# Optimization experiments

Measured on AMD Instinct MI355X. Metric: run time of the kernel, lower is better.

The kernel has to match this reference:

```python
import jax, jax.numpy as jnp
import numpy as np

B, T, D, H = 4, 3072, 1024, 16
HD = D // H

def setup_inputs() -> dict:
    key = jax.random.key(0)
    ks = jax.random.split(key, 7)
    s = 1.0 / np.sqrt(D)
    x = jax.random.normal(ks[0], (B, T, D), dtype=jnp.float32)
    Wq = jax.random.normal(ks[1], (D, D), dtype=jnp.float32) * s
    Wk = jax.random.normal(ks[2], (D, D), dtype=jnp.float32) * s
    Wv = jax.random.normal(ks[3], (D, D), dtype=jnp.float32) * s
    Wo = jax.random.normal(ks[4], (D, D), dtype=jnp.float32) * s
    bo = jnp.zeros((D,), dtype=jnp.float32)
    Wconv = jax.random.normal(ks[5], (D, D, 3), dtype=jnp.float32) * (1.0 / np.sqrt(3 * D))  # (out, in, kw)
    return {"x": x, "Wq": Wq, "Wk": Wk, "Wv": Wv, "Wo": Wo, "bo": bo, "Wconv": Wconv}

def reference(x, Wq, Wk, Wv, Wo, bo, Wconv):
    b, t, d = x.shape
    # stride-3 conv pooling of K/V stream (Conv1d(D, D, 3, stride=3, bias=False))
    kc = jax.lax.conv_general_dilated(
        x.transpose(0, 2, 1), Wconv, window_strides=(3,), padding='VALID',
        dimension_numbers=('NCH', 'OIH', 'NCH')).transpose(0, 2, 1)  # (B, T//3, D)
    k_tmp = jnp.concatenate([x[:, :1, :], kc], axis=1)  # (B, Tk, D)
    tk = k_tmp.shape[1]
    # comparison-based bias mask: masked where 3*k_idx >= q_idx + 0.001
    q_idx = jnp.arange(t, dtype=jnp.float32)
    k_idx = jnp.arange(tk, dtype=jnp.float32)
    mask = (k_idx[None, :] * 3.0 >= q_idx[:, None] + 0.001).astype(x.dtype)  # (T, Tk)
    # projections (torch Linear: y = x @ W.T)
    q = x @ Wq.T
    k = k_tmp @ Wk.T
    v = k_tmp @ Wv.T
    q = q.reshape(b, t, H, HD).transpose(0, 2, 1, 3)   # (B, H, T, HD)
    k = k.reshape(b, tk, H, HD).transpose(0, 2, 1, 3)  # (B, H, Tk, HD)
    v = v.reshape(b, tk, H, HD).transpose(0, 2, 1, 3)
    scores = jnp.einsum('bhqd,bhkd->bhqk', q, k) * (HD ** -0.5)
    scores = scores + mask * jnp.asarray(-1e9, dtype=x.dtype)
    p = jax.nn.softmax(scores, axis=-1)  # dropout is identity in eval (p=0)
    o = jnp.einsum('bhqk,bhkd->bhqd', p, v)
    o = o.transpose(0, 2, 1, 3).reshape(b, t, d)
    return o @ Wo.T + bo
```

## Files before the change

kernel.cpp:

```cpp
#include <hip/hip_runtime.h>
#include <hip/hip_bf16.h>
#include <cstdint>
#include <cstddef>

typedef __attribute__((ext_vector_type(8))) __bf16 bf16x8;
typedef __attribute__((ext_vector_type(4))) __bf16 bf16x4;
typedef __attribute__((ext_vector_type(4))) float  floatx4;

#define MFMA16x16x32(a, b, c) __builtin_amdgcn_mfma_f32_16x16x32_bf16((a), (b), (c), 0, 0, 0)

#define ATTN_SC 0.18033688011112042f

__device__ __forceinline__ void gload_lds16(const void* g, void* l) {
  __builtin_amdgcn_global_load_lds((const __attribute__((address_space(1))) void*)g,
                                   (__attribute__((address_space(3))) void*)l,
                                   16, 0, 0);
}


__global__ void prep_kernel(const float* __restrict__ x,
                            const float* __restrict__ Wq, const float* __restrict__ Wk,
                            const float* __restrict__ Wv, const float* __restrict__ Wo,
                            const float* __restrict__ Wconv,
                            __bf16* __restrict__ xb,
                            __bf16* __restrict__ wqb, __bf16* __restrict__ wkb,
                            __bf16* __restrict__ wvb, __bf16* __restrict__ wob,
                            __bf16* __restrict__ wc2, __bf16* __restrict__ ktmp) {
  const int bid = blockIdx.x, tid = threadIdx.x;
  if (bid < 4096) {
    const int which = bid >> 10;
    const float* src = (which == 0) ? Wq : (which == 1) ? Wk : (which == 2) ? Wv : Wo;
    __bf16* dst = (which == 0) ? wqb : (which == 1) ? wkb : (which == 2) ? wvb : wob;
    const int i = (bid & 1023) * 256 + tid;
    floatx4 v = *(const floatx4*)(src + (size_t)i * 4);
    bf16x4 o; o[0] = (__bf16)v[0]; o[1] = (__bf16)v[1]; o[2] = (__bf16)v[2]; o[3] = (__bf16)v[3];
    *(bf16x4*)(dst + (size_t)i * 4) = o;
  } else if (bid < 5120) {
    const int t = (bid - 4096) * 256 + tid;
    const int o = t >> 8, c = t & 255;
    const float* base = Wconv + (size_t)o * 3072 + c * 12;
    float f[12];
    *(floatx4*)(f)     = *(const floatx4*)(base);
    *(floatx4*)(f + 4) = *(const floatx4*)(base + 4);
    *(floatx4*)(f + 8) = *(const floatx4*)(base + 8);
#pragma unroll
    for (int kw = 0; kw < 3; ++kw) {
      bf16x4 q;
#pragma unroll
      for (int j = 0; j < 4; ++j) q[j] = (__bf16)f[3 * j + kw];
      *(bf16x4*)(wc2 + (size_t)o * 3072 + kw * 1024 + c * 4) = q;
    }
  } else if (bid < 5136) {
    const int i = (bid - 5120) * 256 + tid;
    const int b = i >> 10, c = i & 1023;
    ktmp[(size_t)b * 1025 * 1024 + c] = (__bf16)x[(size_t)b * 3072 * 1024 + c];
  } else {
    const int i = (bid - 5136) * 256 + tid;
    floatx4 v = *(const floatx4*)(x + (size_t)i * 4);
    bf16x4 o; o[0] = (__bf16)v[0]; o[1] = (__bf16)v[1]; o[2] = (__bf16)v[2]; o[3] = (__bf16)v[3];
    *(bf16x4*)(xb + (size_t)i * 4) = o;
  }
}

__global__ void vtrans_kernel(const __bf16* __restrict__ V, __bf16* __restrict__ Vt) {
  __shared__ __attribute__((aligned(16))) __bf16 tile[64][72];
  const int tid = threadIdx.x;
  const int bh = blockIdx.y;
  const int b = bh >> 4, h = bh & 15;
  const int t0 = blockIdx.x * 64;
  const int r = tid >> 3, s = tid & 7;
#pragma unroll
  for (int p = 0; p < 2; ++p) {
    const int t = p * 32 + r;
    bf16x8 v = *(const bf16x8*)(V + ((size_t)(b * 1025 + t0 + t)) * 1024 + h * 64 + s * 8);
    *(bf16x8*)(&tile[t][s * 8]) = v;
  }
  __syncthreads();
#pragma unroll
  for (int p = 0; p < 2; ++p) {
    const int d = p * 32 + r;
    bf16x8 o;
#pragma unroll
    for (int e = 0; e < 8; ++e) o[e] = tile[s * 8 + e][d];
    *(bf16x8*)(Vt + ((size_t)bh * 64 + d) * 1024 + t0 + s * 8) = o;
  }
}


template <int MODE>
__device__ __forceinline__ void gemm4_body(
    const __bf16* __restrict__ A, const __bf16* __restrict__ Bw, void* __restrict__ Cout,
    const float* __restrict__ bias, int N, int K, int m0, int n0,
    __bf16* As, __bf16* Bs)
{
  const int tid  = threadIdx.x;
  const int wave = tid >> 6;
  const int lane = tid & 63;
  const int g    = lane >> 4;
  const int ln   = lane & 15;
  const int wc   = wave * 64;

  size_t aSrcv[2], bSrcv[4];
#pragma unroll
  for (int q = 0; q < 2; ++q) {
    const int c = tid + q * 256, pr = c >> 3, ca = (c & 7) ^ (pr & 7);
    aSrcv[q] = (size_t)(m0 + pr + ((ca >> 2) << 6)) * K + ((ca & 3) << 3);
  }
#pragma unroll
  for (int q = 0; q < 4; ++q) {
    const int c = tid + q * 256, pr = c >> 3, ca = (c & 7) ^ (pr & 7);
    bSrcv[q] = (size_t)(n0 + pr + ((ca >> 2) << 7)) * K + ((ca & 3) << 3);
  }

  int aOff[8], bOff[4];
#pragma unroll
  for (int i = 0; i < 8; ++i) {
    const int ra = i * 16 + ln;
    const int pr = ra & 63;
    const int c  = ((ra >> 6) << 2) + g;
    aOff[i] = pr * 64 + ((c ^ (pr & 7)) << 3);
  }
#pragma unroll
  for (int j = 0; j < 4; ++j) {
    const int rb = wc + j * 16 + ln;
    const int pr = rb & 127;
    const int c  = ((rb >> 7) << 2) + g;
    bOff[j] = pr * 64 + ((c ^ (pr & 7)) << 3);
  }

  floatx4 acc[8][4];
#pragma unroll
  for (int i = 0; i < 8; ++i)
#pragma unroll
    for (int j = 0; j < 4; ++j) { floatx4 z = {0.f, 0.f, 0.f, 0.f}; acc[i][j] = z; }

  auto STAGE = [&](int t, int s) {
    const int koff = t * 32;
    __bf16* ad = As + s * 4096 + (tid << 3);
    __bf16* bd = Bs + s * 8192 + (tid << 3);
    gload_lds16(A  + aSrcv[0] + koff, ad);
    gload_lds16(A  + aSrcv[1] + koff, ad + 2048);
    gload_lds16(Bw + bSrcv[0] + koff, bd);
    gload_lds16(Bw + bSrcv[1] + koff, bd + 2048);
    gload_lds16(Bw + bSrcv[2] + koff, bd + 4096);
    gload_lds16(Bw + bSrcv[3] + koff, bd + 6144);
  };

  bf16x8 af[8], bf[4];

#define READF(s)                                                                   \
  {                                                                                \
    const __bf16* ah_ = As + (s) * 4096;                                           \
    const __bf16* bh_ = Bs + (s) * 8192;                                           \
    _Pragma("unroll")                                                              \
    for (int i_ = 0; i_ < 8; ++i_) af[i_] = *(const bf16x8*)(ah_ + aOff[i_]);      \
    _Pragma("unroll")                                                              \
    for (int j_ = 0; j_ < 4; ++j_) bf[j_] = *(const bf16x8*)(bh_ + bOff[j_]);      \
  }

#define MFMAC()                                                                    \
  {                                                                                \
    __builtin_amdgcn_s_setprio(1);                                                 \
    _Pragma("unroll")                                                              \
    for (int i_ = 0; i_ < 8; ++i_)                                                 \
      _Pragma("unroll")                                                            \
      for (int j_ = 0; j_ < 4; ++j_)                                               \
        acc[i_][j_] = MFMA16x16x32(af[i_], bf[j_], acc[i_][j_]);                   \
    __builtin_amdgcn_s_setprio(0);                                                 \
  }

  const int HT = K >> 5;

  STAGE(0, 0);
  STAGE(1, 1);
  asm volatile("s_waitcnt vmcnt(6)" ::: "memory");
  __builtin_amdgcn_s_barrier();
  __builtin_amdgcn_sched_barrier(0);

  int sp = 0;
  for (int h = 0; h < HT; ++h) {
    const int s2 = (sp + 2 >= 3) ? sp - 1 : sp + 2;
    READF(sp);
    if (h + 2 < HT) STAGE(h + 2, s2);
    MFMAC();
    if (h + 1 < HT) {
      if (h + 2 < HT) { asm volatile("s_waitcnt vmcnt(6) lgkmcnt(0)" ::: "memory"); }
      else            { asm volatile("s_waitcnt vmcnt(0) lgkmcnt(0)" ::: "memory"); }
      __builtin_amdgcn_s_barrier();
      __builtin_amdgcn_sched_barrier(0);
    }
    sp = (sp + 1 >= 3) ? 0 : sp + 1;
  }

#undef READF
#undef MFMAC

#pragma unroll
  for (int j = 0; j < 4; ++j) {
    const int col = n0 + wc + j * 16 + ln;
    float bj = 0.f;
    if (MODE == 2) bj = bias[col];
#pragma unroll
    for (int i = 0; i < 8; ++i)
#pragma unroll
      for (int r = 0; r < 4; ++r) {
        const int row = m0 + i * 16 + g * 4 + r;
        if (MODE == 2) {
          ((float*)Cout)[(size_t)row * N + col] = acc[i][j][r] + bj;
        } else if (MODE == 1) {
          const size_t orow = (size_t)(row >> 10) * 1025 + 1 + (row & 1023);
          ((__bf16*)Cout)[orow * 1024 + col] = (__bf16)acc[i][j][r];
        } else if (MODE == 4) {
          ((__bf16*)Cout)[(size_t)row * N + col] = (__bf16)(acc[i][j][r] * ATTN_SC);
        } else {
          ((__bf16*)Cout)[(size_t)row * N + col] = (__bf16)acc[i][j][r];
        }
      }
  }
}

__global__ __launch_bounds__(256, 2) void gemm_convq_kernel(
    const __bf16* __restrict__ xb, const __bf16* __restrict__ wc2,
    const __bf16* __restrict__ wqb, __bf16* __restrict__ ktmp, __bf16* __restrict__ qb)
{
  __shared__ __attribute__((aligned(16))) __bf16 As[12288];
  __shared__ __attribute__((aligned(16))) __bf16 Bs[24576];
  const int xcd = blockIdx.x & 7, s = blockIdx.x >> 3;
  if (s < 16) {
    const int id = xcd * 16 + s;
    gemm4_body<1>(xb, wc2, ktmp, nullptr, 1024, 3072, (id >> 2) * 128, (id & 3) * 256, As, Bs);
  } else {
    const int id = xcd * 48 + (s - 16);
    gemm4_body<4>(xb, wqb, qb, nullptr, 1024, 1024, (id >> 2) * 128, (id & 3) * 256, As, Bs);
  }
}

__global__ __launch_bounds__(256, 2) void gemm_kv_kernel(
    const __bf16* __restrict__ ktmp, const __bf16* __restrict__ wkb,
    const __bf16* __restrict__ wvb, __bf16* __restrict__ kb, __bf16* __restrict__ vb)
{
  __shared__ __attribute__((aligned(16))) __bf16 As[12288];
  __shared__ __attribute__((aligned(16))) __bf16 Bs[24576];
  const int id = (blockIdx.x & 7) * 33 + (blockIdx.x >> 3);
  const int p  = (id >= 132) ? 1 : 0;
  const int rest = id - p * 132;
  gemm4_body<0>(ktmp, p ? wvb : wkb, p ? vb : kb, nullptr, 1024, 1024,
                (rest >> 2) * 128, (rest & 3) * 256, As, Bs);
}

__global__ __launch_bounds__(256, 2) void gemm_o_kernel(
    const __bf16* __restrict__ ob, const __bf16* __restrict__ wob,
    float* __restrict__ out, const float* __restrict__ bo)
{
  __shared__ __attribute__((aligned(16))) __bf16 As[12288];
  __shared__ __attribute__((aligned(16))) __bf16 Bs[24576];
  const int id = (blockIdx.x & 7) * 48 + (blockIdx.x >> 3);
  gemm4_body<2>(ob, wob, out, bo, 1024, 1024, (id >> 2) * 128, (id & 3) * 256, As, Bs);
}


__global__ __launch_bounds__(256) void attn_kernel(
    const __bf16* __restrict__ Q, const __bf16* __restrict__ Kk,
    const __bf16* __restrict__ Vt, __bf16* __restrict__ O)
{
  __shared__ __attribute__((aligned(16))) __bf16 Kd[2][64 * 64];
  __shared__ __attribute__((aligned(16))) __bf16 Vd[2][64 * 64];
  __shared__ __attribute__((aligned(16))) __bf16 Ps[4][32 * 64];

  const int tid  = threadIdx.x;
  const int wave = tid >> 6;
  const int lane = tid & 63;
  const int g    = lane >> 4;
  const int ln   = lane & 15;

  const int l    = blockIdx.x;
  const int xcd  = l & 7;
  const int b    = xcd >> 1;
  const int rest = l >> 3;
  const int h    = rest & 15;
  const int qt   = ((11 - (rest >> 4)) << 1) | (xcd & 1);
  const int q0   = qt * 128 + wave * 32;

  const size_t qrow0 = (size_t)b * 3072 + q0;
  const size_t krow0 = (size_t)b * 1025;
  const size_t vtrow = ((size_t)(b * 16 + h)) * 64;
  const int hc = h * 64;
  const int sw = (ln & 7) << 3;
  __bf16* Pw = Ps[wave];

  const int srow = lane >> 3;
  const int scol = (lane & 7) * 8;

  auto stage = [&](int kt, int bb) {
    const int kb0 = kt * 64;
#pragma unroll
    for (int i = 0; i < 2; ++i) {
      const int rr = (wave * 2 + i) * 8 + srow;
      gload_lds16(Kk + (krow0 + kb0 + rr) * 1024 + hc + scol,
                  Kd[bb] + (size_t)rr * 64 + scol);
      gload_lds16(Vt + (vtrow + rr) * 1024 + kb0 + scol,
                  Vd[bb] + (size_t)rr * 64 + scol);
    }
  };

  bf16x8 qf[2][2];
#pragma unroll
  for (int i = 0; i < 2; ++i)
#pragma unroll
    for (int kc = 0; kc < 2; ++kc)
      qf[i][kc] = *(const bf16x8*)(Q + (qrow0 + i * 16 + ln) * 1024 + hc + kc * 32 + g * 8);

  floatx4 oacc[2][4];
  floatx4 oal[2];
#pragma unroll
  for (int i = 0; i < 2; ++i) {
    floatx4 z = {0.f, 0.f, 0.f, 0.f};
    oal[i] = z;
#pragma unroll
    for (int dt = 0; dt < 4; ++dt) oacc[i][dt] = z;
  }

  bf16x8 ones;
#pragma unroll
  for (int e = 0; e < 8; ++e) ones[e] = (__bf16)1.0f;

  const int nkt_blk = (((qt * 128 + 127) / 3) >> 6) + 1;
  const int nfull   = (q0 >= 189) ? ((q0 - 189) / 192 + 1) : 0;

  stage(0, 0);

  for (int kt = 0; kt < nkt_blk; ++kt) {
    const int bb = kt & 1;
    __syncthreads();
    if (kt + 1 < nkt_blk) stage(kt + 1, bb ^ 1);
    const int kb0 = kt * 64;
    const bool masked = (kt >= nfull);

    bf16x8 kf[4][2];
#pragma unroll
    for (int jk = 0; jk < 4; ++jk)
#pragma unroll
      for (int kc = 0; kc < 2; ++kc)
        kf[jk][kc] = *(const bf16x8*)(Kd[bb] + (jk * 16 + ln) * 64 + kc * 32 + g * 8);

#pragma unroll
    for (int jk = 0; jk < 4; ++jk)
#pragma unroll
      for (int i = 0; i < 2; ++i) {
        floatx4 s = {0.f, 0.f, 0.f, 0.f};
        s = MFMA16x16x32(kf[jk][0], qf[i][0], s);
        s = MFMA16x16x32(kf[jk][1], qf[i][1], s);
        float p[4];
#pragma unroll
        for (int r = 0; r < 4; ++r) {
          float e = __builtin_amdgcn_exp2f(s[r]);
          if (masked) {
            const int key = kb0 + jk * 16 + 4 * g + r;
            const int q   = q0 + i * 16 + ln;
            e = (3 * key <= q) ? e : 0.f;
          }
          p[r] = e;
        }
        bf16x4 pk;
        pk[0] = (__bf16)p[0]; pk[1] = (__bf16)p[1]; pk[2] = (__bf16)p[2]; pk[3] = (__bf16)p[3];
        *(bf16x4*)(Pw + (i * 16 + ln) * 64 + ((jk * 16 + 4 * g) ^ sw)) = pk;
      }

#pragma unroll
    for (int kc = 0; kc < 2; ++kc) {
      bf16x8 pf0 = *(const bf16x8*)(Pw + (ln) * 64      + ((kc * 32 + g * 8) ^ sw));
      bf16x8 pf1 = *(const bf16x8*)(Pw + (16 + ln) * 64 + ((kc * 32 + g * 8) ^ sw));
      oal[0] = MFMA16x16x32(ones, pf0, oal[0]);
      oal[1] = MFMA16x16x32(ones, pf1, oal[1]);
#pragma unroll
      for (int dt = 0; dt < 4; ++dt) {
        bf16x8 vf = *(const bf16x8*)(Vd[bb] + (dt * 16 + ln) * 64 + kc * 32 + g * 8);
        oacc[0][dt] = MFMA16x16x32(vf, pf0, oacc[0][dt]);
        oacc[1][dt] = MFMA16x16x32(vf, pf1, oacc[1][dt]);
      }
    }
  }

#pragma unroll
  for (int i = 0; i < 2; ++i) {
    const float inv = 1.0f / oal[i][0];
    const size_t row = qrow0 + i * 16 + ln;
#pragma unroll
    for (int dt = 0; dt < 4; ++dt) {
      bf16x4 o4;
#pragma unroll
      for (int r = 0; r < 4; ++r) o4[r] = (__bf16)(oacc[i][dt][r] * inv);
      *(bf16x4*)(O + row * 1024 + hc + dt * 16 + 4 * g) = o4;
    }
  }
}


extern "C" void kernel_launch(void* const* d_in, const int* in_sizes, int n_in,
                              void* d_out, int out_size, void* d_ws, size_t ws_size,
                              hipStream_t stream) {
  (void)in_sizes; (void)n_in; (void)out_size; (void)ws_size;
  const float* x     = (const float*)d_in[0];
  const float* Wq    = (const float*)d_in[1];
  const float* Wk    = (const float*)d_in[2];
  const float* Wv    = (const float*)d_in[3];
  const float* Wo    = (const float*)d_in[4];
  const float* bo    = (const float*)d_in[5];
  const float* Wconv = (const float*)d_in[6];

  char* ws = (char*)d_ws;
  const size_t SZ_XQ = (size_t)12288 * 1024 * 2;
  const size_t SZ_KT = (size_t)4224 * 1024 * 2;
  const size_t SZ_W  = (size_t)1024 * 1024 * 2;

  __bf16* xb   = (__bf16*)(ws);
  __bf16* qb   = (__bf16*)(ws + SZ_XQ);
  __bf16* ktmp = (__bf16*)(ws + 2 * SZ_XQ);
  __bf16* kb   = (__bf16*)(ws + 2 * SZ_XQ + SZ_KT);
  __bf16* vb   = (__bf16*)(ws + 2 * SZ_XQ + 2 * SZ_KT);
  __bf16* wqb  = (__bf16*)(ws + 2 * SZ_XQ + 3 * SZ_KT);
  __bf16* wkb  = (__bf16*)(ws + 2 * SZ_XQ + 3 * SZ_KT + SZ_W);
  __bf16* wvb  = (__bf16*)(ws + 2 * SZ_XQ + 3 * SZ_KT + 2 * SZ_W);
  __bf16* wob  = (__bf16*)(ws + 2 * SZ_XQ + 3 * SZ_KT + 3 * SZ_W);
  __bf16* wc2  = (__bf16*)(ws + 2 * SZ_XQ + 3 * SZ_KT + 4 * SZ_W);
  __bf16* vt   = xb;

  prep_kernel<<<dim3(17424), dim3(256), 0, stream>>>(x, Wq, Wk, Wv, Wo, Wconv,
                                                     xb, wqb, wkb, wvb, wob, wc2, ktmp);
  gemm_convq_kernel<<<dim3(512), dim3(256), 0, stream>>>(xb, wc2, wqb, ktmp, qb);
  gemm_kv_kernel<<<dim3(264), dim3(256), 0, stream>>>(ktmp, wkb, wvb, kb, vb);
  vtrans_kernel<<<dim3(16, 64), dim3(256), 0, stream>>>(vb, vt);
  attn_kernel<<<dim3(1536), dim3(256), 0, stream>>>(qb, kb, vt, qb);
  gemm_o_kernel<<<dim3(384), dim3(256), 0, stream>>>(qb, wob, (float*)d_out, bo);
}
```

Before: 314.4 us.

## Split conv GEMM K dimension across taps with fp16 partials and reduction

The stride-3 conv GEMM (K=3072) is split into three K=1024 slices, one per tap, so 384 blocks do equal work alongside the 384 Q-projection blocks instead of 128 long blocks. Two taps write fp16 partial sums into reused K/V buffers, and a new reduce kernel adds them into the third tap's bf16 output in ktmp. This targets load imbalance and tail effects in the fused conv+Q launch. The cost is an extra kernel launch, extra memory traffic for the partials, and some rounding from storing partials in fp16 and bf16.

```diff
diff --git a/kernel.cpp b/kernel.cpp
--- a/kernel.cpp
+++ b/kernel.cpp
@@ -5,6 +5,7 @@
 
 typedef __attribute__((ext_vector_type(8))) __bf16 bf16x8;
 typedef __attribute__((ext_vector_type(4))) __bf16 bf16x4;
+typedef __attribute__((ext_vector_type(8))) _Float16 halfx8;
 typedef __attribute__((ext_vector_type(4))) float  floatx4;
 
 #define MFMA16x16x32(a, b, c) __builtin_amdgcn_mfma_f32_16x16x32_bf16((a), (b), (c), 0, 0, 0)
@@ -90,7 +91,7 @@
 template <int MODE>
 __device__ __forceinline__ void gemm4_body(
     const __bf16* __restrict__ A, const __bf16* __restrict__ Bw, void* __restrict__ Cout,
-    const float* __restrict__ bias, int N, int K, int m0, int n0,
+    const float* __restrict__ bias, int lda, int ldb, int K, int m0, int n0,
     __bf16* As, __bf16* Bs)
 {
   const int tid  = threadIdx.x;
@@ -104,12 +105,12 @@
 #pragma unroll
   for (int q = 0; q < 2; ++q) {
     const int c = tid + q * 256, pr = c >> 3, ca = (c & 7) ^ (pr & 7);
-    aSrcv[q] = (size_t)(m0 + pr + ((ca >> 2) << 6)) * K + ((ca & 3) << 3);
+    aSrcv[q] = (size_t)(m0 + pr + ((ca >> 2) << 6)) * lda + ((ca & 3) << 3);
   }
 #pragma unroll
   for (int q = 0; q < 4; ++q) {
     const int c = tid + q * 256, pr = c >> 3, ca = (c & 7) ^ (pr & 7);
-    bSrcv[q] = (size_t)(n0 + pr + ((ca >> 2) << 7)) * K + ((ca & 3) << 3);
+    bSrcv[q] = (size_t)(n0 + pr + ((ca >> 2) << 7)) * ldb + ((ca & 3) << 3);
   }
 
   int aOff[8], bOff[4];
@@ -206,14 +207,16 @@
       for (int r = 0; r < 4; ++r) {
         const int row = m0 + i * 16 + g * 4 + r;
         if (MODE == 2) {
-          ((float*)Cout)[(size_t)row * N + col] = acc[i][j][r] + bj;
+          ((float*)Cout)[(size_t)row * 1024 + col] = acc[i][j][r] + bj;
         } else if (MODE == 1) {
           const size_t orow = (size_t)(row >> 10) * 1025 + 1 + (row & 1023);
           ((__bf16*)Cout)[orow * 1024 + col] = (__bf16)acc[i][j][r];
         } else if (MODE == 4) {
-          ((__bf16*)Cout)[(size_t)row * N + col] = (__bf16)(acc[i][j][r] * ATTN_SC);
+          ((__bf16*)Cout)[(size_t)row * 1024 + col] = (__bf16)(acc[i][j][r] * ATTN_SC);
+        } else if (MODE == 5) {
+          ((_Float16*)Cout)[(size_t)row * 1024 + col] = (_Float16)acc[i][j][r];
         } else {
-          ((__bf16*)Cout)[(size_t)row * N + col] = (__bf16)acc[i][j][r];
+          ((__bf16*)Cout)[(size_t)row * 1024 + col] = (__bf16)acc[i][j][r];
         }
       }
   }
@@ -221,18 +224,45 @@
 
 __global__ __launch_bounds__(256, 2) void gemm_convq_kernel(
     const __bf16* __restrict__ xb, const __bf16* __restrict__ wc2,
-    const __bf16* __restrict__ wqb, __bf16* __restrict__ ktmp, __bf16* __restrict__ qb)
+    const __bf16* __restrict__ wqb, __bf16* __restrict__ ktmp, __bf16* __restrict__ qb,
+    _Float16* __restrict__ P0, _Float16* __restrict__ P1)
 {
   __shared__ __attribute__((aligned(16))) __bf16 As[12288];
   __shared__ __attribute__((aligned(16))) __bf16 Bs[24576];
   const int xcd = blockIdx.x & 7, s = blockIdx.x >> 3;
-  if (s < 16) {
-    const int id = xcd * 16 + s;
-    gemm4_body<1>(xb, wc2, ktmp, nullptr, 1024, 3072, (id >> 2) * 128, (id & 3) * 256, As, Bs);
+  if (s < 48) {
+    const int id = xcd * 48 + s;
+    const int tap = id >> 7, tl = id & 127;
+    const int m0 = (tl >> 2) * 128, n0 = (tl & 3) * 256;
+    const __bf16* Ac = xb  + tap * 1024;
+    const __bf16* Bc = wc2 + tap * 1024;
+    if (tap == 2)
+      gemm4_body<1>(Ac, Bc, ktmp, nullptr, 3072, 3072, 1024, m0, n0, As, Bs);
+    else if (tap == 1)
+      gemm4_body<5>(Ac, Bc, P1, nullptr, 3072, 3072, 1024, m0, n0, As, Bs);
+    else
+      gemm4_body<5>(Ac, Bc, P0, nullptr, 3072, 3072, 1024, m0, n0, As, Bs);
   } else {
-    const int id = xcd * 48 + (s - 16);
-    gemm4_body<4>(xb, wqb, qb, nullptr, 1024, 1024, (id >> 2) * 128, (id & 3) * 256, As, Bs);
-  }
+    const int id = xcd * 48 + (s - 48);
+    gemm4_body<4>(xb, wqb, qb, nullptr, 1024, 1024, 1024,
+                  (id >> 2) * 128, (id & 3) * 256, As, Bs);
+  }
+}
+
+__global__ void reduce_conv_kernel(const _Float16* __restrict__ P0, const _Float16* __restrict__ P1,
+                                   __bf16* __restrict__ ktmp) {
+  const int idx = blockIdx.x * 256 + threadIdx.x;
+  const int r = idx >> 7;
+  const int c = (idx & 127) * 8;
+  const size_t orow = (size_t)(r >> 10) * 1025 + 1 + (r & 1023);
+  __bf16* kp = ktmp + orow * 1024 + c;
+  bf16x8 k8 = *(const bf16x8*)kp;
+  halfx8 p0 = *(const halfx8*)(P0 + (size_t)r * 1024 + c);
+  halfx8 p1 = *(const halfx8*)(P1 + (size_t)r * 1024 + c);
+  bf16x8 o;
+#pragma unroll
+  for (int e = 0; e < 8; ++e) o[e] = (__bf16)((float)k8[e] + (float)p0[e] + (float)p1[e]);
+  *(bf16x8*)kp = o;
 }
 
 __global__ __launch_bounds__(256, 2) void gemm_kv_kernel(
@@ -244,7 +274,7 @@
   const int id = (blockIdx.x & 7) * 33 + (blockIdx.x >> 3);
   const int p  = (id >= 132) ? 1 : 0;
   const int rest = id - p * 132;
-  gemm4_body<0>(ktmp, p ? wvb : wkb, p ? vb : kb, nullptr, 1024, 1024,
+  gemm4_body<0>(ktmp, p ? wvb : wkb, p ? vb : kb, nullptr, 1024, 1024, 1024,
                 (rest >> 2) * 128, (rest & 3) * 256, As, Bs);
 }
 
@@ -255,7 +285,7 @@
   __shared__ __attribute__((aligned(16))) __bf16 As[12288];
   __shared__ __attribute__((aligned(16))) __bf16 Bs[24576];
   const int id = (blockIdx.x & 7) * 48 + (blockIdx.x >> 3);
-  gemm4_body<2>(ob, wob, out, bo, 1024, 1024, (id >> 2) * 128, (id & 3) * 256, As, Bs);
+  gemm4_body<2>(ob, wob, out, bo, 1024, 1024, 1024, (id >> 2) * 128, (id & 3) * 256, As, Bs);
 }
 
 
@@ -425,9 +455,13 @@
   __bf16* wc2  = (__bf16*)(ws + 2 * SZ_XQ + 3 * SZ_KT + 4 * SZ_W);
   __bf16* vt   = xb;
 
+  _Float16* P0 = (_Float16*)kb;
+  _Float16* P1 = (_Float16*)vb;
+
   prep_kernel<<<dim3(17424), dim3(256), 0, stream>>>(x, Wq, Wk, Wv, Wo, Wconv,
                                                      xb, wqb, wkb, wvb, wob, wc2, ktmp);
-  gemm_convq_kernel<<<dim3(512), dim3(256), 0, stream>>>(xb, wc2, wqb, ktmp, qb);
+  gemm_convq_kernel<<<dim3(768), dim3(256), 0, stream>>>(xb, wc2, wqb, ktmp, qb, P0, P1);
+  reduce_conv_kernel<<<dim3(2048), dim3(256), 0, stream>>>(P0, P1, ktmp);
   gemm_kv_kernel<<<dim3(264), dim3(256), 0, stream>>>(ktmp, wkb, wvb, kb, vb);
   vtrans_kernel<<<dim3(16, 64), dim3(256), 0, stream>>>(vb, vt);
   attn_kernel<<<dim3(1536), dim3(256), 0, stream>>>(qb, kb, vt, qb);
```

New measurement: 318.7 us. About the same (+1.4%).

## Load GEMM B-operand fragments directly from global into registers, drop B LDS staging

Applied to the files above, without the earlier changes.

The shared GEMM body no longer stages the weight (B) tile through LDS. Each lane now loads its own B fragments straight from global memory into registers with inline global_load_dwordx4, double-buffered across two k-steps, while A stays on the LDS pipeline. This removes the LDS traffic and footprint for B (freeing LDS for occupancy) but gives up sharing B across waves, since each wave loads only its own 64 columns, and it adds register pressure and hand-tuned vmcnt waits. The loop assumes an even number of k-steps.

```diff
diff --git a/kernel.cpp b/kernel.cpp
--- a/kernel.cpp
+++ b/kernel.cpp
@@ -91,7 +91,7 @@
 __device__ __forceinline__ void gemm4_body(
     const __bf16* __restrict__ A, const __bf16* __restrict__ Bw, void* __restrict__ Cout,
     const float* __restrict__ bias, int N, int K, int m0, int n0,
-    __bf16* As, __bf16* Bs)
+    __bf16* As)
 {
   const int tid  = threadIdx.x;
   const int wave = tid >> 6;
@@ -100,19 +100,14 @@
   const int ln   = lane & 15;
   const int wc   = wave * 64;
 
-  size_t aSrcv[2], bSrcv[4];
+  size_t aSrcv[2];
 #pragma unroll
   for (int q = 0; q < 2; ++q) {
     const int c = tid + q * 256, pr = c >> 3, ca = (c & 7) ^ (pr & 7);
     aSrcv[q] = (size_t)(m0 + pr + ((ca >> 2) << 6)) * K + ((ca & 3) << 3);
   }
-#pragma unroll
-  for (int q = 0; q < 4; ++q) {
-    const int c = tid + q * 256, pr = c >> 3, ca = (c & 7) ^ (pr & 7);
-    bSrcv[q] = (size_t)(n0 + pr + ((ca >> 2) << 7)) * K + ((ca & 3) << 3);
-  }
-
-  int aOff[8], bOff[4];
+
+  int aOff[8];
 #pragma unroll
   for (int i = 0; i < 8; ++i) {
     const int ra = i * 16 + ln;
@@ -120,13 +115,11 @@
     const int c  = ((ra >> 6) << 2) + g;
     aOff[i] = pr * 64 + ((c ^ (pr & 7)) << 3);
   }
-#pragma unroll
-  for (int j = 0; j < 4; ++j) {
-    const int rb = wc + j * 16 + ln;
-    const int pr = rb & 127;
-    const int c  = ((rb >> 7) << 2) + g;
-    bOff[j] = pr * 64 + ((c ^ (pr & 7)) << 3);
-  }
+
+  unsigned long long baddr[4];
+#pragma unroll
+  for (int j = 0; j < 4; ++j)
+    baddr[j] = (unsigned long long)(Bw + (size_t)(n0 + wc + j * 16 + ln) * K) + g * 16;
 
   floatx4 acc[8][4];
 #pragma unroll
@@ -137,54 +130,75 @@
   auto STAGE = [&](int t, int s) {
     const int koff = t * 32;
     __bf16* ad = As + s * 4096 + (tid << 3);
-    __bf16* bd = Bs + s * 8192 + (tid << 3);
-    gload_lds16(A  + aSrcv[0] + koff, ad);
-    gload_lds16(A  + aSrcv[1] + koff, ad + 2048);
-    gload_lds16(Bw + bSrcv[0] + koff, bd);
-    gload_lds16(Bw + bSrcv[1] + koff, bd + 2048);
-    gload_lds16(Bw + bSrcv[2] + koff, bd + 4096);
-    gload_lds16(Bw + bSrcv[3] + koff, bd + 6144);
+    gload_lds16(A + aSrcv[0] + koff, ad);
+    gload_lds16(A + aSrcv[1] + koff, ad + 2048);
   };
 
-  bf16x8 af[8], bf[4];
+  floatx4 bE[4], bO[4];
+  bf16x8 af[8];
+
+#define LOADB(DST)                                                                 \
+  {                                                                                \
+    _Pragma("unroll")                                                              \
+    for (int j_ = 0; j_ < 4; ++j_)                                                 \
+      asm volatile("global_load_dwordx4 %0, %1, off"                               \
+                   : "=&v"(DST[j_]) : "v"(baddr[j_]));                             \
+    _Pragma("unroll")                                                              \
+    for (int j_ = 0; j_ < 4; ++j_) baddr[j_] += 64;                                \
+  }
 
 #define READF(s)                                                                   \
   {                                                                                \
     const __bf16* ah_ = As + (s) * 4096;                                           \
-    const __bf16* bh_ = Bs + (s) * 8192;                                           \
     _Pragma("unroll")                                                              \
     for (int i_ = 0; i_ < 8; ++i_) af[i_] = *(const bf16x8*)(ah_ + aOff[i_]);      \
-    _Pragma("unroll")                                                              \
-    for (int j_ = 0; j_ < 4; ++j_) bf[j_] = *(const bf16x8*)(bh_ + bOff[j_]);      \
-  }
-
-#define MFMAC()                                                                    \
+  }
+
+#define MFMAC(BF)                                                                  \
   {                                                                                \
     __builtin_amdgcn_s_setprio(1);                                                 \
     _Pragma("unroll")                                                              \
     for (int i_ = 0; i_ < 8; ++i_)                                                 \
       _Pragma("unroll")                                                            \
       for (int j_ = 0; j_ < 4; ++j_)                                               \
-        acc[i_][j_] = MFMA16x16x32(af[i_], bf[j_], acc[i_][j_]);                   \
+        acc[i_][j_] = MFMA16x16x32(af[i_], __builtin_bit_cast(bf16x8, BF[j_]),     \
+                                   acc[i_][j_]);                                   \
     __builtin_amdgcn_s_setprio(0);                                                 \
   }
 
   const int HT = K >> 5;
 
+  LOADB(bE);
   STAGE(0, 0);
   STAGE(1, 1);
-  asm volatile("s_waitcnt vmcnt(6)" ::: "memory");
+  asm volatile("s_waitcnt vmcnt(2)" ::: "memory");
   __builtin_amdgcn_s_barrier();
   __builtin_amdgcn_sched_barrier(0);
 
   int sp = 0;
-  for (int h = 0; h < HT; ++h) {
-    const int s2 = (sp + 2 >= 3) ? sp - 1 : sp + 2;
+  for (int h = 0; h < HT; h += 2) {
     READF(sp);
-    if (h + 2 < HT) STAGE(h + 2, s2);
-    MFMAC();
-    if (h + 1 < HT) {
-      if (h + 2 < HT) { asm volatile("s_waitcnt vmcnt(6) lgkmcnt(0)" ::: "memory"); }
+    LOADB(bO);
+    {
+      const int s2 = (sp + 2 >= 3) ? sp - 1 : sp + 2;
+      if (h + 2 < HT) STAGE(h + 2, s2);
+    }
+    MFMAC(bE);
+    if (h + 2 < HT) { asm volatile("s_waitcnt vmcnt(2) lgkmcnt(0)" ::: "memory"); }
+    else            { asm volatile("s_waitcnt vmcnt(0) lgkmcnt(0)" ::: "memory"); }
+    __builtin_amdgcn_s_barrier();
+    __builtin_amdgcn_sched_barrier(0);
+    sp = (sp + 1 >= 3) ? 0 : sp + 1;
+
+    READF(sp);
+    if (h + 2 < HT) LOADB(bE);
+    {
+      const int s2 = (sp + 2 >= 3) ? sp - 1 : sp + 2;
+      if (h + 3 < HT) STAGE(h + 3, s2);
+    }
+    MFMAC(bO);
+    if (h + 2 < HT) {
+      if (h + 3 < HT) { asm volatile("s_waitcnt vmcnt(2) lgkmcnt(0)" ::: "memory"); }
       else            { asm volatile("s_waitcnt vmcnt(0) lgkmcnt(0)" ::: "memory"); }
       __builtin_amdgcn_s_barrier();
       __builtin_amdgcn_sched_barrier(0);
@@ -192,6 +206,7 @@
     sp = (sp + 1 >= 3) ? 0 : sp + 1;
   }
 
+#undef LOADB
 #undef READF
 #undef MFMAC
 
@@ -224,14 +239,13 @@
     const __bf16* __restrict__ wqb, __bf16* __restrict__ ktmp, __bf16* __restrict__ qb)
 {
   __shared__ __attribute__((aligned(16))) __bf16 As[12288];
-  __shared__ __attribute__((aligned(16))) __bf16 Bs[24576];
   const int xcd = blockIdx.x & 7, s = blockIdx.x >> 3;
   if (s < 16) {
     const int id = xcd * 16 + s;
-    gemm4_body<1>(xb, wc2, ktmp, nullptr, 1024, 3072, (id >> 2) * 128, (id & 3) * 256, As, Bs);
+    gemm4_body<1>(xb, wc2, ktmp, nullptr, 1024, 3072, (id >> 2) * 128, (id & 3) * 256, As);
   } else {
     const int id = xcd * 48 + (s - 16);
-    gemm4_body<4>(xb, wqb, qb, nullptr, 1024, 1024, (id >> 2) * 128, (id & 3) * 256, As, Bs);
+    gemm4_body<4>(xb, wqb, qb, nullptr, 1024, 1024, (id >> 2) * 128, (id & 3) * 256, As);
   }
 }
 
@@ -240,12 +254,11 @@
     const __bf16* __restrict__ wvb, __bf16* __restrict__ kb, __bf16* __restrict__ vb)
 {
   __shared__ __attribute__((aligned(16))) __bf16 As[12288];
-  __shared__ __attribute__((aligned(16))) __bf16 Bs[24576];
   const int id = (blockIdx.x & 7) * 33 + (blockIdx.x >> 3);
   const int p  = (id >= 132) ? 1 : 0;
   const int rest = id - p * 132;
   gemm4_body<0>(ktmp, p ? wvb : wkb, p ? vb : kb, nullptr, 1024, 1024,
-                (rest >> 2) * 128, (rest & 3) * 256, As, Bs);
+                (rest >> 2) * 128, (rest & 3) * 256, As);
 }
 
 __global__ __launch_bounds__(256, 2) void gemm_o_kernel(
@@ -253,9 +266,8 @@
     float* __restrict__ out, const float* __restrict__ bo)
 {
   __shared__ __attribute__((aligned(16))) __bf16 As[12288];
-  __shared__ __attribute__((aligned(16))) __bf16 Bs[24576];
   const int id = (blockIdx.x & 7) * 48 + (blockIdx.x >> 3);
-  gemm4_body<2>(ob, wob, out, bo, 1024, 1024, (id >> 2) * 128, (id & 3) * 256, As, Bs);
+  gemm4_body<2>(ob, wob, out, bo, 1024, 1024, (id >> 2) * 128, (id & 3) * 256, As);
 }
 
 
```

Result: slower. 354.8 us (+12.8%).
